# Kernel optimization log

Hardware: AMD Instinct MI355X
Metric: run time of the kernel (lower is better)

The kernel has to match this reference:

```python
import jax, jax.numpy as jnp
import numpy as np

ALPHA = 0.2          # LeakyReLU negative slope
NEG_INF = -9e15      # mask value from the original code


def setup_inputs() -> dict:
    key = jax.random.key(0)
    k1, k2, k3, k4 = jax.random.split(key, 4)
    B, N, F_in, F_out = 8, 2048, 64, 64
    x = jax.random.normal(k1, (B, N, F_in), dtype=jnp.float32)
    adj = jax.random.randint(k2, (B, N, N), 0, 2, dtype=jnp.int32)
    W = jax.random.normal(k3, (F_in, F_out), dtype=jnp.float32)
    a = jax.random.normal(k4, (2 * F_out, 1), dtype=jnp.float32)
    return {"x": x, "adj": adj, "W": W, "a": a}


def reference(x, adj, W, a):
    # h: [B, N, F_out]
    h = jnp.matmul(x, W)
    F_out = W.shape[1]
    a1 = a[:F_out, 0]   # source half of attention vector
    a2 = a[F_out:, 0]   # target half
    # e_ij = leakyrelu(h_i . a1 + h_j . a2)  -- identical math to the
    # original cat([h_i, h_j]) @ a without materializing [B,N*N,2F].
    s1 = jnp.einsum('bnf,f->bn', h, a1)  # [B, N]
    s2 = jnp.einsum('bnf,f->bn', h, a2)  # [B, N]
    e = jax.nn.leaky_relu(s1[:, :, None] + s2[:, None, :], negative_slope=ALPHA)
    masked = jnp.where(adj > 0, e, NEG_INF)
    attention = jax.nn.softmax(masked, axis=2)  # [B, N, N]
    # dropout p=0.0 / eval mode -> identity
    h_prime = jnp.matmul(attention, h)          # [B, N, F_out]
    return jax.nn.elu(h_prime)                  # concat=True branch
```

## Files before the change

kernel.cpp:

```cpp
#include <hip/hip_runtime.h>
#include <cstdint>

#define LRELU_ALPHA 0.2f
#define NEG_INF -9000000000000000.0f
#define L2E 1.4426950408889634f

typedef __bf16 bf16x8 __attribute__((ext_vector_type(8)));
typedef float floatx4 __attribute__((ext_vector_type(4)));
typedef unsigned int uintx4 __attribute__((ext_vector_type(4)));

constexpr int Bb = 8, Nn = 2048, Ff = 64;
constexpr int TJ = 64;
constexpr int SEGW = 8;
constexpr int SLICE = Nn / SEGW;
constexpr int NT = SLICE / TJ;
constexpr int NROWS = Bb * Nn;

__device__ __forceinline__ unsigned short f2bf(float f) {
    unsigned u = __builtin_bit_cast(unsigned, f);
    u = u + 0x7FFFu + ((u >> 16) & 1u);
    return (unsigned short)(u >> 16);
}

__device__ __forceinline__ unsigned cvt_pk_bf16(float lo, float hi) {
    unsigned r;
    asm("v_cvt_pk_bf16_f32 %0, %1, %2" : "=v"(r) : "v"(lo), "v"(hi));
    return r;
}

__global__ __launch_bounds__(256) void gat_prep(
    const float* __restrict__ x, const float* __restrict__ W, const float* __restrict__ a,
    unsigned short* __restrict__ hT, float* __restrict__ s1g, float* __restrict__ s2g)
{
    constexpr int STR2 = 36;
    __shared__ unsigned short hblk[64 * STR2];
    const int tid = threadIdx.x;
    const int blk = blockIdx.x;
    const int b  = blk >> 6;
    const int i0 = (blk & 63) * 32;
    const int w    = tid >> 6;
    const int lane = tid & 63;

    float wcol[64];
    #pragma unroll
    for (int k = 0; k < 64; ++k) wcol[k] = W[k * 64 + lane];
    const float a1 = a[lane], a2 = a[64 + lane];

    for (int r = 0; r < 8; ++r) {
        const int il = w * 8 + r;
        const int i  = i0 + il;
        const float* xrow = x + ((size_t)(b * Nn + i)) * 64;
        float h0 = 0.f, h1 = 0.f, h2 = 0.f, h3 = 0.f;
        #pragma unroll
        for (int k = 0; k < 64; k += 4) {
            h0 = fmaf(xrow[k],     wcol[k],     h0);
            h1 = fmaf(xrow[k + 1], wcol[k + 1], h1);
            h2 = fmaf(xrow[k + 2], wcol[k + 2], h2);
            h3 = fmaf(xrow[k + 3], wcol[k + 3], h3);
        }
        const float h = (h0 + h1) + (h2 + h3);
        float p1 = h * a1, p2 = h * a2;
        #pragma unroll
        for (int off = 32; off; off >>= 1) {
            p1 += __shfl_xor(p1, off);
            p2 += __shfl_xor(p2, off);
        }
        if (lane == 0) { s1g[b * Nn + i] = p1; s2g[b * Nn + i] = p2; }
        hblk[lane * STR2 + il] = f2bf(h);
    }
    __syncthreads();
    {
        const int f = tid >> 2, c = (tid & 3) * 8;
        uint4 v = *reinterpret_cast<const uint4*>(&hblk[f * STR2 + c]);
        *reinterpret_cast<uint4*>(hT + ((size_t)b * 64 + f) * Nn + i0 + c) = v;
    }
}

__global__ __launch_bounds__(512, 6) void gat_attn(
    const int* __restrict__ adj, const unsigned short* __restrict__ hT,
    const float* __restrict__ s1g, const float* __restrict__ s2g,
    float* __restrict__ out)
{
    __shared__ float O_lds[SEGW][16][65];
    __shared__ float m_lds[SEGW][16];
    __shared__ float l_lds[SEGW][16];

    const int tid  = threadIdx.x;
    const int blk  = blockIdx.x;
    const int b    = blk >> 7;
    const int i0   = (blk & 127) * 16;
    const int s    = tid >> 6;
    const int lane = tid & 63;
    const int fl   = lane & 15;
    const int q    = lane >> 4;

    const int i = i0 + fl;
    const float s1v = s1g[b * Nn + i];
    const int* adj_row = adj + ((size_t)(b * Nn + i)) * Nn + s * SLICE;
    const unsigned short* hTb = hT + (size_t)b * 64 * Nn + s * SLICE;
    const float* s2b = s2g + b * Nn + s * SLICE;

    float m = NEG_INF, l = 0.f;
    floatx4 C[4] = {};

    for (int jt = 0; jt < NT; ++jt) {
        const int jloc = jt * TJ;

        int4 adjv[4];
        {
            const int* arow = adj_row + jloc;
            const int4* ap0 = reinterpret_cast<const int4*>(arow + q * 8);
            adjv[0] = ap0[0]; adjv[1] = ap0[1];
            const int4* ap1 = reinterpret_cast<const int4*>(arow + 32 + q * 8);
            adjv[2] = ap1[0]; adjv[3] = ap1[1];
        }

        float p[16];
        const int* av = reinterpret_cast<const int*>(adjv);
        #pragma unroll
        for (int tt = 0; tt < 2; ++tt) {
            float s2v[8];
            *reinterpret_cast<float4*>(&s2v[0]) =
                *reinterpret_cast<const float4*>(&s2b[jloc + tt * 32 + q * 8]);
            *reinterpret_cast<float4*>(&s2v[4]) =
                *reinterpret_cast<const float4*>(&s2b[jloc + tt * 32 + q * 8 + 4]);
            #pragma unroll
            for (int jj = 0; jj < 8; ++jj) {
                float ev = s1v + s2v[jj];
                ev = fmaxf(ev, LRELU_ALPHA * ev);
                p[tt * 8 + jj] = (av[tt * 8 + jj] > 0) ? ev : NEG_INF;
            }
        }
        float tmax = p[0];
        #pragma unroll
        for (int k = 1; k < 16; ++k) tmax = fmaxf(tmax, p[k]);
        tmax = fmaxf(tmax, __shfl_xor(tmax, 16));
        tmax = fmaxf(tmax, __shfl_xor(tmax, 32));
        const float m_new = fmaxf(m, tmax);

        if (__any(m_new > m)) {
            const float alpha_s = exp2f((m - m_new) * L2E);
            l *= alpha_s;
            float ac[4];
            #pragma unroll
            for (int r = 0; r < 4; ++r) ac[r] = __shfl(alpha_s, q * 4 + r);
            #pragma unroll
            for (int u = 0; u < 4; ++u)
                #pragma unroll
                for (int r = 0; r < 4; ++r) C[u][r] *= ac[r];
            m = m_new;
        }

        float tsum = 0.f;
        #pragma unroll
        for (int k = 0; k < 16; ++k) {
            p[k] = exp2f((p[k] - m) * L2E);
            tsum += p[k];
        }
        tsum += __shfl_xor(tsum, 16);
        tsum += __shfl_xor(tsum, 32);
        l += tsum;

        uintx4 pa, pb;
        #pragma unroll
        for (int d = 0; d < 4; ++d) {
            pa[d] = cvt_pk_bf16(p[2 * d],     p[2 * d + 1]);
            pb[d] = cvt_pk_bf16(p[8 + 2 * d], p[8 + 2 * d + 1]);
        }
        const bf16x8 A0 = __builtin_bit_cast(bf16x8, pa);
        const bf16x8 A1 = __builtin_bit_cast(bf16x8, pb);

        __builtin_amdgcn_s_setprio(1);
        #pragma unroll
        for (int u = 0; u < 4; ++u) {
            const bf16x8 B0 = *reinterpret_cast<const bf16x8*>(
                hTb + (size_t)(u * 16 + fl) * Nn + jloc + q * 8);
            C[u] = __builtin_amdgcn_mfma_f32_16x16x32_bf16(A0, B0, C[u], 0, 0, 0);
            const bf16x8 B1 = *reinterpret_cast<const bf16x8*>(
                hTb + (size_t)(u * 16 + fl) * Nn + jloc + 32 + q * 8);
            C[u] = __builtin_amdgcn_mfma_f32_16x16x32_bf16(A1, B1, C[u], 0, 0, 0);
        }
        __builtin_amdgcn_s_setprio(0);
    }

    #pragma unroll
    for (int u = 0; u < 4; ++u)
        #pragma unroll
        for (int r = 0; r < 4; ++r)
            O_lds[s][q * 4 + r][u * 16 + fl] = C[u][r];
    if (q == 0) { m_lds[s][fl] = m; l_lds[s][fl] = l; }
    __syncthreads();

    const int row = tid >> 5;
    const int f0  = (tid & 31) * 2;

    float mv[SEGW];
    #pragma unroll
    for (int k = 0; k < SEGW; ++k) mv[k] = m_lds[k][row];
    float mstar = mv[0];
    #pragma unroll
    for (int k = 1; k < SEGW; ++k) mstar = fmaxf(mstar, mv[k]);

    float lsum = 0.f, acc0 = 0.f, acc1 = 0.f;
    #pragma unroll
    for (int k = 0; k < SEGW; ++k) {
        const float wgt = exp2f((mv[k] - mstar) * L2E);
        lsum += l_lds[k][row] * wgt;
        const float2 ov = *reinterpret_cast<const float2*>(&O_lds[k][row][f0]);
        acc0 += ov.x * wgt;
        acc1 += ov.y * wgt;
    }
    const float inv = 1.f / lsum;
    float v0 = acc0 * inv, v1 = acc1 * inv;
    v0 = (v0 > 0.f) ? v0 : (exp2f(v0 * L2E) - 1.f);
    v1 = (v1 > 0.f) ? v1 : (exp2f(v1 * L2E) - 1.f);
    float2 o2; o2.x = v0; o2.y = v1;
    *reinterpret_cast<float2*>(&out[((size_t)(b * Nn + i0 + row)) * 64 + f0]) = o2;
}

extern "C" void kernel_launch(void* const* d_in, const int* in_sizes, int n_in,
                              void* d_out, int out_size, void* d_ws, size_t ws_size,
                              hipStream_t stream) {
    const float* x   = (const float*)d_in[0];
    const int*   adj = (const int*)d_in[1];
    const float* W   = (const float*)d_in[2];
    const float* a   = (const float*)d_in[3];
    float* out = (float*)d_out;

    char* p = (char*)d_ws;
    unsigned short* hT = (unsigned short*)p;  p += (size_t)Bb * 64 * Nn * sizeof(unsigned short);
    float* s1 = (float*)p;                    p += (size_t)NROWS * sizeof(float);
    float* s2 = (float*)p;

    gat_prep<<<dim3(Bb * Nn / 32), dim3(256), 0, stream>>>(x, W, a, hT, s1, s2);
    gat_attn<<<dim3(NROWS / 16), dim3(512), 0, stream>>>(adj, hT, s1, s2, out);
}
```

Measured before the change: 244.0 us.

## Pack adjacency into bitmasks in a separate kernel and prefetch attention operands

```diff
diff --git a/kernel.cpp b/kernel.cpp
--- a/kernel.cpp
+++ b/kernel.cpp
@@ -15,6 +15,7 @@
 constexpr int SLICE = Nn / SEGW;
 constexpr int NT = SLICE / TJ;
 constexpr int NROWS = Bb * Nn;
+constexpr int MCH = Nn / 64;
 
 __device__ __forceinline__ unsigned short f2bf(float f) {
     unsigned u = __builtin_bit_cast(unsigned, f);
@@ -26,6 +27,35 @@
     unsigned r;
     asm("v_cvt_pk_bf16_f32 %0, %1, %2" : "=v"(r) : "v"(lo), "v"(hi));
     return r;
+}
+
+__global__ __launch_bounds__(256) void gat_pack(
+    const int* __restrict__ adj, unsigned long long* __restrict__ masks)
+{
+    const int wid  = blockIdx.x * 4 + (threadIdx.x >> 6);
+    const int lane = threadIdx.x & 63;
+    #pragma unroll
+    for (int rr = 0; rr < 2; ++rr) {
+        const int row = wid * 2 + rr;
+        const int* ar = adj + (size_t)row * Nn;
+        unsigned long long acc = 0;
+        #pragma unroll
+        for (int cb = 0; cb < 8; ++cb) {
+            int v0 = ar[(cb * 4 + 0) * 64 + lane];
+            int v1 = ar[(cb * 4 + 1) * 64 + lane];
+            int v2 = ar[(cb * 4 + 2) * 64 + lane];
+            int v3 = ar[(cb * 4 + 3) * 64 + lane];
+            unsigned long long m0 = __ballot(v0 > 0);
+            unsigned long long m1 = __ballot(v1 > 0);
+            unsigned long long m2 = __ballot(v2 > 0);
+            unsigned long long m3 = __ballot(v3 > 0);
+            if (lane == cb * 4 + 0) acc = m0;
+            if (lane == cb * 4 + 1) acc = m1;
+            if (lane == cb * 4 + 2) acc = m2;
+            if (lane == cb * 4 + 3) acc = m3;
+        }
+        if (lane < 32) masks[(size_t)row * MCH + lane] = acc;
+    }
 }
 
 __global__ __launch_bounds__(256) void gat_prep(
@@ -76,8 +106,8 @@
     }
 }
 
-__global__ __launch_bounds__(512, 6) void gat_attn(
-    const int* __restrict__ adj, const unsigned short* __restrict__ hT,
+__global__ __launch_bounds__(512, 4) void gat_attn(
+    const unsigned long long* __restrict__ masks, const unsigned short* __restrict__ hT,
     const float* __restrict__ s1g, const float* __restrict__ s2g,
     float* __restrict__ out)
 {
@@ -96,41 +126,59 @@
 
     const int i = i0 + fl;
     const float s1v = s1g[b * Nn + i];
-    const int* adj_row = adj + ((size_t)(b * Nn + i)) * Nn + s * SLICE;
     const unsigned short* hTb = hT + (size_t)b * 64 * Nn + s * SLICE;
     const float* s2b = s2g + b * Nn + s * SLICE;
+    const unsigned long long* mrow = masks + (size_t)(b * Nn + i) * MCH + s * NT;
 
     float m = NEG_INF, l = 0.f;
     floatx4 C[4] = {};
 
+    unsigned long long mk = mrow[0];
+    float4 sA = *reinterpret_cast<const float4*>(&s2b[q * 8]);
+    float4 sB = *reinterpret_cast<const float4*>(&s2b[q * 8 + 4]);
+    float4 sC = *reinterpret_cast<const float4*>(&s2b[32 + q * 8]);
+    float4 sD = *reinterpret_cast<const float4*>(&s2b[32 + q * 8 + 4]);
+
+    #pragma unroll
     for (int jt = 0; jt < NT; ++jt) {
         const int jloc = jt * TJ;
 
-        int4 adjv[4];
+        bf16x8 Bv[8];
+        #pragma unroll
+        for (int u = 0; u < 4; ++u) {
+            Bv[2 * u] = *reinterpret_cast<const bf16x8*>(
+                hTb + (size_t)(u * 16 + fl) * Nn + jloc + q * 8);
+            Bv[2 * u + 1] = *reinterpret_cast<const bf16x8*>(
+                hTb + (size_t)(u * 16 + fl) * Nn + jloc + 32 + q * 8);
+        }
+
+        const int jn = (jt + 1 < NT) ? jloc + TJ : jloc;
+        const unsigned long long mk_n = mrow[(jt + 1 < NT) ? jt + 1 : jt];
+        float4 nA = *reinterpret_cast<const float4*>(&s2b[jn + q * 8]);
+        float4 nB = *reinterpret_cast<const float4*>(&s2b[jn + q * 8 + 4]);
+        float4 nC = *reinterpret_cast<const float4*>(&s2b[jn + 32 + q * 8]);
+        float4 nD = *reinterpret_cast<const float4*>(&s2b[jn + 32 + q * 8 + 4]);
+
+        const unsigned blo = ((unsigned)mk >> (q * 8)) & 0xFFu;
+        const unsigned bhi = ((unsigned)(mk >> 32) >> (q * 8)) & 0xFFu;
+        float p[16];
         {
-            const int* arow = adj_row + jloc;
-            const int4* ap0 = reinterpret_cast<const int4*>(arow + q * 8);
-            adjv[0] = ap0[0]; adjv[1] = ap0[1];
-            const int4* ap1 = reinterpret_cast<const int4*>(arow + 32 + q * 8);
-            adjv[2] = ap1[0]; adjv[3] = ap1[1];
-        }
-
-        float p[16];
-        const int* av = reinterpret_cast<const int*>(adjv);
-        #pragma unroll
-        for (int tt = 0; tt < 2; ++tt) {
-            float s2v[8];
-            *reinterpret_cast<float4*>(&s2v[0]) =
-                *reinterpret_cast<const float4*>(&s2b[jloc + tt * 32 + q * 8]);
-            *reinterpret_cast<float4*>(&s2v[4]) =
-                *reinterpret_cast<const float4*>(&s2b[jloc + tt * 32 + q * 8 + 4]);
+            const float s2v0[8] = { sA.x, sA.y, sA.z, sA.w, sB.x, sB.y, sB.z, sB.w };
+            const float s2v1[8] = { sC.x, sC.y, sC.z, sC.w, sD.x, sD.y, sD.z, sD.w };
             #pragma unroll
             for (int jj = 0; jj < 8; ++jj) {
-                float ev = s1v + s2v[jj];
+                float ev = s1v + s2v0[jj];
                 ev = fmaxf(ev, LRELU_ALPHA * ev);
-                p[tt * 8 + jj] = (av[tt * 8 + jj] > 0) ? ev : NEG_INF;
+                p[jj] = (blo & (1u << jj)) ? ev : NEG_INF;
             }
-        }
+            #pragma unroll
+            for (int jj = 0; jj < 8; ++jj) {
+                float ev = s1v + s2v1[jj];
+                ev = fmaxf(ev, LRELU_ALPHA * ev);
+                p[8 + jj] = (bhi & (1u << jj)) ? ev : NEG_INF;
+            }
+        }
+
         float tmax = p[0];
         #pragma unroll
         for (int k = 1; k < 16; ++k) tmax = fmaxf(tmax, p[k]);
@@ -173,14 +221,12 @@
         __builtin_amdgcn_s_setprio(1);
         #pragma unroll
         for (int u = 0; u < 4; ++u) {
-            const bf16x8 B0 = *reinterpret_cast<const bf16x8*>(
-                hTb + (size_t)(u * 16 + fl) * Nn + jloc + q * 8);
-            C[u] = __builtin_amdgcn_mfma_f32_16x16x32_bf16(A0, B0, C[u], 0, 0, 0);
-            const bf16x8 B1 = *reinterpret_cast<const bf16x8*>(
-                hTb + (size_t)(u * 16 + fl) * Nn + jloc + 32 + q * 8);
-            C[u] = __builtin_amdgcn_mfma_f32_16x16x32_bf16(A1, B1, C[u], 0, 0, 0);
+            C[u] = __builtin_amdgcn_mfma_f32_16x16x32_bf16(A0, Bv[2 * u],     C[u], 0, 0, 0);
+            C[u] = __builtin_amdgcn_mfma_f32_16x16x32_bf16(A1, Bv[2 * u + 1], C[u], 0, 0, 0);
         }
         __builtin_amdgcn_s_setprio(0);
+
+        mk = mk_n; sA = nA; sB = nB; sC = nC; sD = nD;
     }
 
     #pragma unroll
@@ -230,8 +276,10 @@
     char* p = (char*)d_ws;
     unsigned short* hT = (unsigned short*)p;  p += (size_t)Bb * 64 * Nn * sizeof(unsigned short);
     float* s1 = (float*)p;                    p += (size_t)NROWS * sizeof(float);
-    float* s2 = (float*)p;
-
+    float* s2 = (float*)p;                    p += (size_t)NROWS * sizeof(float);
+    unsigned long long* masks = (unsigned long long*)p;
+
+    gat_pack<<<dim3(NROWS / 8), dim3(256), 0, stream>>>(adj, masks);
     gat_prep<<<dim3(Bb * Nn / 32), dim3(256), 0, stream>>>(x, W, a, hT, s1, s2);
-    gat_attn<<<dim3(NROWS / 16), dim3(512), 0, stream>>>(adj, hT, s1, s2, out);
-}
+    gat_attn<<<dim3(NROWS / 16), dim3(512), 0, stream>>>(masks, hT, s1, s2, out);
+}
```

Result: slower. 253.5 us (+3.9%).
